# Kernel tuning notes

Measured on AMD Instinct MI355X. Metric: run time of the kernel, lower is better.

Reference implementation:

```python
import jax, jax.numpy as jnp
import numpy as np


def setup_inputs() -> dict:
    key = jax.random.key(0)
    k1, k2, k3 = jax.random.split(key, 3)
    B, D, L = 16384, 1024, 4
    x = jax.random.normal(k1, (B, D), dtype=jnp.float32)
    weights = jax.random.normal(k2, (L, D, 1), dtype=jnp.float32)
    biases = jax.random.normal(k3, (L, D, 1), dtype=jnp.float32)
    return {"x": x, "weights": weights, "biases": biases}


def reference(x, weights, biases):
    # DCN cross layer. Literal torch math per layer:
    #   out = (x[:,:,None] @ out[:,None,:] @ w_i + b_i).squeeze(-1) + out
    # Algebraically identical (associativity of matmul):
    #   out = x * (out @ w_i) + b_i.T + out
    w = weights[..., 0]  # (L, D)
    b = biases[..., 0]   # (L, D)

    def step(out, wb):
        w_i, b_i = wb
        s = out @ w_i  # (B,) scalar per row: out . w_i
        out = x * s[:, None] + b_i[None, :] + out
        return out, None

    out, _ = jax.lax.scan(step, x, (w, b))
    return out
```

## Files before the change

kernel.cpp:

```cpp
#include <hip/hip_runtime.h>


typedef float v4f __attribute__((ext_vector_type(4)));

constexpr int D  = 1024;
constexpr int D4 = D / 4;
constexpr int L  = 4;
constexpr int WAVES_PER_BLOCK = 4;
constexpr int ROWS_PER_WAVE   = 4;
constexpr int ROWS_PER_BLOCK  = WAVES_PER_BLOCK * ROWS_PER_WAVE;
constexpr int NRED = 4 * L + 3;

template<int CTRL>
__device__ __forceinline__ float dpp_add(float v) {
    int t = __builtin_amdgcn_update_dpp(0, __float_as_int(v), CTRL, 0xF, 0xF, true);
    return v + __int_as_float(t);
}

__device__ __forceinline__ float wave_sum(float v) {
    v = dpp_add<0x111>(v);
    v = dpp_add<0x112>(v);
    v = dpp_add<0x114>(v);
    v = dpp_add<0x118>(v);
    v = dpp_add<0x142>(v);
    v = dpp_add<0x143>(v);
    return __int_as_float(__builtin_amdgcn_readlane(__float_as_int(v), 63));
}

__device__ __forceinline__ float hsum(v4f a) { return (a.x + a.y) + (a.z + a.w); }

__global__ __launch_bounds__(256, 4) void cross_layer_kernel(
    const float* __restrict__ x,
    const float* __restrict__ w,
    const float* __restrict__ b,
    float* __restrict__ out,
    int B)
{
    __shared__ v4f sw [L * D4];
    __shared__ v4f spb[L * D4];

    const int tid  = threadIdx.x;
    const int lane = tid & 63;
    const int wave = tid >> 6;
    const int row0 = blockIdx.x * ROWS_PER_BLOCK + wave * ROWS_PER_WAVE;

    const v4f* w4 = reinterpret_cast<const v4f*>(w);
    const v4f* b4 = reinterpret_cast<const v4f*>(b);
    v4f wt[L], bt[L];
    #pragma unroll
    for (int l = 0; l < L; ++l) wt[l] = w4[l * D4 + tid];
    #pragma unroll
    for (int l = 0; l < L; ++l) bt[l] = b4[l * D4 + tid];

    v4f xr[ROWS_PER_WAVE][4];
    const v4f* x4 = reinterpret_cast<const v4f*>(x) + (size_t)row0 * D4;
    #pragma unroll
    for (int r = 0; r < ROWS_PER_WAVE; ++r) {
        if (row0 + r < B) {
            #pragma unroll
            for (int c = 0; c < 4; ++c)
                xr[r][c] = __builtin_nontemporal_load(&x4[r * D4 + lane + c * 64]);
        } else {
            #pragma unroll
            for (int c = 0; c < 4; ++c) xr[r][c] = (v4f)(0.f);
        }
    }

    {
        v4f p = (v4f)(0.f);
        #pragma unroll
        for (int l = 0; l < L; ++l) {
            sw[l * D4 + tid] = wt[l];
            p += bt[l];
            spb[l * D4 + tid] = p;
        }
    }
    __syncthreads();

    float red[NRED];
    #pragma unroll
    for (int l = 0; l < L; ++l) {
        v4f wl[4];
        #pragma unroll
        for (int c = 0; c < 4; ++c)
            wl[c] = sw[l * D4 + lane + c * 64];

        if (l >= 1) {
            v4f ea = spb[(l - 1) * D4 + lane] * wl[0];
            #pragma unroll
            for (int c = 1; c < 4; ++c)
                ea += spb[(l - 1) * D4 + lane + c * 64] * wl[c];
            red[4 * L + l - 1] = hsum(ea);
        }

        #pragma unroll
        for (int r = 0; r < ROWS_PER_WAVE; ++r) {
            v4f a = xr[r][0] * wl[0];
            #pragma unroll
            for (int c = 1; c < 4; ++c)
                a += xr[r][c] * wl[c];
            red[r * 4 + l] = hsum(a);
        }
    }

    #pragma unroll
    for (int k = 0; k < NRED; ++k)
        red[k] = wave_sum(red[k]);

    float A[ROWS_PER_WAVE];
    #pragma unroll
    for (int r = 0; r < ROWS_PER_WAVE; ++r) {
        float a = 1.f + red[r * 4 + 0];
        a = a + a * red[r * 4 + 1] + red[4 * L + 0];
        a = a + a * red[r * 4 + 2] + red[4 * L + 1];
        a = a + a * red[r * 4 + 3] + red[4 * L + 2];
        A[r] = a;
    }

    v4f* o4 = reinterpret_cast<v4f*>(out) + (size_t)row0 * D4;
    #pragma unroll
    for (int c = 0; c < 4; ++c) {
        const v4f cs = spb[(L - 1) * D4 + lane + c * 64];
        #pragma unroll
        for (int r = 0; r < ROWS_PER_WAVE; ++r) {
            if (row0 + r < B) {
                v4f v = xr[r][c] * A[r] + cs;
                __builtin_nontemporal_store(v, &o4[r * D4 + lane + c * 64]);
            }
        }
    }
}

extern "C" void kernel_launch(void* const* d_in, const int* in_sizes, int n_in,
                              void* d_out, int out_size, void* d_ws, size_t ws_size,
                              hipStream_t stream) {
    const float* x  = (const float*)d_in[0];
    const float* w  = (const float*)d_in[1];
    const float* b  = (const float*)d_in[2];
    float* out      = (float*)d_out;

    const int B = in_sizes[0] / D;
    const int blocks = (B + ROWS_PER_BLOCK - 1) / ROWS_PER_BLOCK;
    cross_layer_kernel<<<blocks, 256, 0, stream>>>(x, w, b, out, B);
}
```

Before: 123.3 us.

## Drop LDS staging, keep weights in registers, and software-pipeline row chunks

Removes the shared-memory staging of weights and prefix-summed biases plus the block barrier. Each wave now loads all weights and biases into registers and computes the bias-dot corrections itself. Rows per wave double to 8 and are processed in chunks of 2, with x loads issued two chunks ahead so memory latency overlaps the dot products, reductions and stores. The occupancy hint in launch bounds is dropped, and the much higher register use (weights, biases, and up to three chunks of x) may lower occupancy. Redundant weight and bias loads per wave also add some L2 traffic.

Result: no change. 121.9 us (-1.1%).

```diff
diff --git a/kernel.cpp b/kernel.cpp
--- a/kernel.cpp
+++ b/kernel.cpp
@@ -7,9 +7,10 @@
 constexpr int D4 = D / 4;
 constexpr int L  = 4;
 constexpr int WAVES_PER_BLOCK = 4;
-constexpr int ROWS_PER_WAVE   = 4;
+constexpr int ROWS_PER_WAVE   = 8;
+constexpr int CHUNK           = 2;
+constexpr int NCH             = ROWS_PER_WAVE / CHUNK;
 constexpr int ROWS_PER_BLOCK  = WAVES_PER_BLOCK * ROWS_PER_WAVE;
-constexpr int NRED = 4 * L + 3;
 
 template<int CTRL>
 __device__ __forceinline__ float dpp_add(float v) {
@@ -29,16 +30,13 @@
 
 __device__ __forceinline__ float hsum(v4f a) { return (a.x + a.y) + (a.z + a.w); }
 
-__global__ __launch_bounds__(256, 4) void cross_layer_kernel(
+__global__ __launch_bounds__(256) void cross_layer_kernel(
     const float* __restrict__ x,
     const float* __restrict__ w,
     const float* __restrict__ b,
     float* __restrict__ out,
     int B)
 {
-    __shared__ v4f sw [L * D4];
-    __shared__ v4f spb[L * D4];
-
     const int tid  = threadIdx.x;
     const int lane = tid & 63;
     const int wave = tid >> 6;
@@ -46,86 +44,115 @@
 
     const v4f* w4 = reinterpret_cast<const v4f*>(w);
     const v4f* b4 = reinterpret_cast<const v4f*>(b);
-    v4f wt[L], bt[L];
+    const v4f* x4 = reinterpret_cast<const v4f*>(x);
+
+    v4f wr[L][4];
     #pragma unroll
-    for (int l = 0; l < L; ++l) wt[l] = w4[l * D4 + tid];
+    for (int l = 0; l < L; ++l)
+        #pragma unroll
+        for (int c = 0; c < 4; ++c)
+            wr[l][c] = w4[l * D4 + lane + c * 64];
+
+    v4f bt[L][4];
     #pragma unroll
-    for (int l = 0; l < L; ++l) bt[l] = b4[l * D4 + tid];
+    for (int l = 0; l < L; ++l)
+        #pragma unroll
+        for (int c = 0; c < 4; ++c)
+            bt[l][c] = b4[l * D4 + lane + c * 64];
 
-    v4f xr[ROWS_PER_WAVE][4];
-    const v4f* x4 = reinterpret_cast<const v4f*>(x) + (size_t)row0 * D4;
+    v4f xb[NCH][CHUNK][4];
     #pragma unroll
-    for (int r = 0; r < ROWS_PER_WAVE; ++r) {
-        if (row0 + r < B) {
+    for (int r = 0; r < CHUNK; ++r) {
+        const int row = row0 + r;
+        if (row < B) {
             #pragma unroll
             for (int c = 0; c < 4; ++c)
-                xr[r][c] = __builtin_nontemporal_load(&x4[r * D4 + lane + c * 64]);
+                xb[0][r][c] = __builtin_nontemporal_load(&x4[(size_t)row * D4 + lane + c * 64]);
         } else {
             #pragma unroll
-            for (int c = 0; c < 4; ++c) xr[r][c] = (v4f)(0.f);
+            for (int c = 0; c < 4; ++c) xb[0][r][c] = (v4f)(0.f);
         }
     }
 
-    {
-        v4f p = (v4f)(0.f);
-        #pragma unroll
-        for (int l = 0; l < L; ++l) {
-            sw[l * D4 + tid] = wt[l];
-            p += bt[l];
-            spb[l * D4 + tid] = p;
-        }
-    }
-    __syncthreads();
-
-    float red[NRED];
+    v4f p[4] = {(v4f)(0.f), (v4f)(0.f), (v4f)(0.f), (v4f)(0.f)};
+    float epart[3];
     #pragma unroll
     for (int l = 0; l < L; ++l) {
-        v4f wl[4];
+        if (l >= 1) {
+            v4f ea = p[0] * wr[l][0];
+            #pragma unroll
+            for (int c = 1; c < 4; ++c) ea += p[c] * wr[l][c];
+            epart[l - 1] = hsum(ea);
+        }
         #pragma unroll
-        for (int c = 0; c < 4; ++c)
-            wl[c] = sw[l * D4 + lane + c * 64];
+        for (int c = 0; c < 4; ++c) p[c] += bt[l][c];
+    }
+    float e1 = wave_sum(epart[0]);
+    float e2 = wave_sum(epart[1]);
+    float e3 = wave_sum(epart[2]);
 
-        if (l >= 1) {
-            v4f ea = spb[(l - 1) * D4 + lane] * wl[0];
+    #pragma unroll
+    for (int r = 0; r < CHUNK; ++r) {
+        const int row = row0 + CHUNK + r;
+        if (row < B) {
             #pragma unroll
-            for (int c = 1; c < 4; ++c)
-                ea += spb[(l - 1) * D4 + lane + c * 64] * wl[c];
-            red[4 * L + l - 1] = hsum(ea);
-        }
-
-        #pragma unroll
-        for (int r = 0; r < ROWS_PER_WAVE; ++r) {
-            v4f a = xr[r][0] * wl[0];
+            for (int c = 0; c < 4; ++c)
+                xb[1][r][c] = __builtin_nontemporal_load(&x4[(size_t)row * D4 + lane + c * 64]);
+        } else {
             #pragma unroll
-            for (int c = 1; c < 4; ++c)
-                a += xr[r][c] * wl[c];
-            red[r * 4 + l] = hsum(a);
+            for (int c = 0; c < 4; ++c) xb[1][r][c] = (v4f)(0.f);
         }
     }
 
     #pragma unroll
-    for (int k = 0; k < NRED; ++k)
-        red[k] = wave_sum(red[k]);
+    for (int k = 0; k < NCH; ++k) {
+        if (k + 2 < NCH) {
+            #pragma unroll
+            for (int r = 0; r < CHUNK; ++r) {
+                const int row = row0 + (k + 2) * CHUNK + r;
+                if (row < B) {
+                    #pragma unroll
+                    for (int c = 0; c < 4; ++c)
+                        xb[k + 2][r][c] = __builtin_nontemporal_load(&x4[(size_t)row * D4 + lane + c * 64]);
+                } else {
+                    #pragma unroll
+                    for (int c = 0; c < 4; ++c) xb[k + 2][r][c] = (v4f)(0.f);
+                }
+            }
+        }
 
-    float A[ROWS_PER_WAVE];
-    #pragma unroll
-    for (int r = 0; r < ROWS_PER_WAVE; ++r) {
-        float a = 1.f + red[r * 4 + 0];
-        a = a + a * red[r * 4 + 1] + red[4 * L + 0];
-        a = a + a * red[r * 4 + 2] + red[4 * L + 1];
-        a = a + a * red[r * 4 + 3] + red[4 * L + 2];
-        A[r] = a;
-    }
+        float dd[CHUNK][L];
+        #pragma unroll
+        for (int r = 0; r < CHUNK; ++r) {
+            #pragma unroll
+            for (int l = 0; l < L; ++l) {
+                v4f a = xb[k][r][0] * wr[l][0];
+                #pragma unroll
+                for (int c = 1; c < 4; ++c)
+                    a += xb[k][r][c] * wr[l][c];
+                dd[r][l] = hsum(a);
+            }
+        }
+        #pragma unroll
+        for (int r = 0; r < CHUNK; ++r)
+            #pragma unroll
+            for (int l = 0; l < L; ++l)
+                dd[r][l] = wave_sum(dd[r][l]);
 
-    v4f* o4 = reinterpret_cast<v4f*>(out) + (size_t)row0 * D4;
-    #pragma unroll
-    for (int c = 0; c < 4; ++c) {
-        const v4f cs = spb[(L - 1) * D4 + lane + c * 64];
         #pragma unroll
-        for (int r = 0; r < ROWS_PER_WAVE; ++r) {
-            if (row0 + r < B) {
-                v4f v = xr[r][c] * A[r] + cs;
-                __builtin_nontemporal_store(v, &o4[r * D4 + lane + c * 64]);
+        for (int r = 0; r < CHUNK; ++r) {
+            const int row = row0 + k * CHUNK + r;
+            if (row < B) {
+                float a = 1.f + dd[r][0];
+                a = a + a * dd[r][1] + e1;
+                a = a + a * dd[r][2] + e2;
+                a = a + a * dd[r][3] + e3;
+                v4f* o4 = reinterpret_cast<v4f*>(out) + (size_t)row * D4;
+                #pragma unroll
+                for (int c = 0; c < 4; ++c) {
+                    v4f v = xb[k][r][c] * a + p[c];
+                    __builtin_nontemporal_store(v, &o4[lane + c * 64]);
+                }
             }
         }
     }
```
